# Kernel optimization log

Hardware: AMD Instinct MI355X
Metric: run time of the kernel (lower is better)

## Reference

```python
import jax, jax.numpy as jnp
import numpy as np

STEPS = 3


def setup_inputs() -> dict:
    key = jax.random.key(0)
    ks = jax.random.split(key, 6)
    N, H, B = 1000000, 128, 16384
    x = jax.random.normal(ks[0], (N, H), dtype=jnp.float32)
    batch_vec = jnp.sort(jax.random.randint(ks[1], (N,), 0, B)).astype(jnp.int64)
    scale_ih = 1.0 / np.sqrt(2 * H)
    scale_hh = 1.0 / np.sqrt(H)
    W_ih = jax.random.normal(ks[2], (4 * H, 2 * H), dtype=jnp.float32) * scale_ih
    W_hh = jax.random.normal(ks[3], (4 * H, H), dtype=jnp.float32) * scale_hh
    b_ih = jnp.zeros((4 * H,), dtype=jnp.float32)
    b_hh = jnp.zeros((4 * H,), dtype=jnp.float32)
    return {"x": x, "batch_vec": batch_vec, "W_ih": W_ih, "W_hh": W_hh,
            "b_ih": b_ih, "b_hh": b_hh, "num_graphs": B}


def _set2set(x, batch_vec, W_ih, W_hh, b_ih, b_hh, B):
    N, H = x.shape
    q_star = jnp.zeros((B, 2 * H), x.dtype)
    h = jnp.zeros((B, H), x.dtype)
    c = jnp.zeros((B, H), x.dtype)
    bias = b_ih + b_hh
    for _ in range(STEPS):
        # LSTMCell (torch gate order: i, f, g, o)
        gates = q_star @ W_ih.T + h @ W_hh.T + bias  # [B, 4H]
        i, f, g, o = jnp.split(gates, 4, axis=-1)
        c = jax.nn.sigmoid(f) * c + jax.nn.sigmoid(i) * jnp.tanh(g)
        h = jax.nn.sigmoid(o) * jnp.tanh(c)
        q = h  # [B, H]
        # attention logits per node
        e = jnp.sum(x * q[batch_vec], axis=-1)  # [N]
        emax = jax.ops.segment_max(e, batch_vec, num_segments=B)
        emax = jax.lax.stop_gradient(jnp.where(jnp.isfinite(emax), emax, 0.0))
        ex = jnp.exp(e - emax[batch_vec])
        denom = jax.ops.segment_sum(ex, batch_vec, num_segments=B)
        a = ex / denom[batch_vec]  # segment softmax, [N]
        r = jax.ops.segment_sum(a[:, None] * x, batch_vec, num_segments=B)  # [B, H]
        q_star = jnp.concatenate([q, r], axis=-1)  # [B, 2H]
    return q_star


def reference(x, batch_vec, W_ih, W_hh, b_ih, b_hh, num_graphs):
    return _set2set(x, batch_vec, W_ih, W_hh, b_ih, b_hh, int(num_graphs))
```

## Files before the change

kernel.cpp:

```cpp
#include <hip/hip_runtime.h>
#include <math.h>

#define HDIM 128
#define G4 512
#define TS 36

typedef float vf4 __attribute__((ext_vector_type(4)));
typedef unsigned short u16x8 __attribute__((ext_vector_type(8)));

__device__ __forceinline__ float sigm(float v) { return 1.0f / (1.0f + __expf(-v)); }
__device__ __forceinline__ float ftanh(float v) {
    return 1.0f - 2.0f / (__expf(2.0f * v) + 1.0f);
}
__device__ __forceinline__ float dot4(vf4 a, vf4 b) {
    return a.x * b.x + a.y * b.y + a.z * b.z + a.w * b.w;
}
__device__ __forceinline__ vf4 ldnt4(const float* p) {
    return __builtin_nontemporal_load((const vf4*)p);
}
__device__ __forceinline__ unsigned short f2bf(float f) {
    unsigned u = __float_as_uint(f);
    u += 0x7fff + ((u >> 16) & 1);
    return (unsigned short)(u >> 16);
}
__device__ __forceinline__ float bf2f(unsigned short h) {
    return __uint_as_float(((unsigned)h) << 16);
}

__global__ __launch_bounds__(256) void k_setup(const float* __restrict__ W_ih,
                                               const float* __restrict__ W_hh,
                                               const int* __restrict__ batch_vec, int N, int B,
                                               float* __restrict__ Wc, int* __restrict__ seg_start) {
    int t = blockIdx.x * 256 + threadIdx.x;
    if (t < G4 * 2 * HDIM) {
        int g = t >> 8;
        int k = t & 255;
        float w = W_ih[g * 256 + k];
        if (k < HDIM) w += W_hh[g * HDIM + k];
        Wc[t] = w;
    }
    if (t <= B) {
        int lo = 0, hi = N;
        while (lo < hi) {
            int mid = (lo + hi) >> 1;
            if (batch_vec[mid] < t) lo = mid + 1; else hi = mid;
        }
        seg_start[t] = lo;
    }
}

__global__ __launch_bounds__(256) void k_head(const float* __restrict__ Wc,
                                              const float* __restrict__ b_ih,
                                              const float* __restrict__ b_hh,
                                              float* __restrict__ gh0) {
    __shared__ float h0s[HDIM];
    int t = threadIdx.x;
    int g = blockIdx.x * 256 + t;
    if (t < HDIM) {
        float bi = b_ih[t] + b_hh[t];
        float bg = b_ih[2 * HDIM + t] + b_hh[2 * HDIM + t];
        float bo = b_ih[3 * HDIM + t] + b_hh[3 * HDIM + t];
        float c0 = sigm(bi) * ftanh(bg);
        h0s[t] = sigm(bo) * ftanh(c0);
    }
    __syncthreads();
    float s = 0.0f;
#pragma unroll
    for (int k = 0; k < HDIM; k += 4) {
        vf4 w = *(const vf4*)(Wc + (size_t)g * 256 + k);
        s += w.x * h0s[k] + w.y * h0s[k + 1] + w.z * h0s[k + 2] + w.w * h0s[k + 3];
    }
    gh0[g] = s;
}

#define UPD(m_, d_, ra_, rb_, p_, xa_, xb_)  \
    {                                        \
        float mn_ = fmaxf(m_, p_);           \
        float sc_ = __expf(m_ - mn_);        \
        float pe_ = __expf(p_ - mn_);        \
        d_ = d_ * sc_ + pe_;                 \
        ra_ = ra_ * sc_ + pe_ * xa_;         \
        rb_ = rb_ * sc_ + pe_ * xb_;         \
        m_ = mn_;                            \
    }

#define SHFL16(p_)                  \
    p_ += __shfl_xor(p_, 1, 64);    \
    p_ += __shfl_xor(p_, 2, 64);    \
    p_ += __shfl_xor(p_, 4, 64);    \
    p_ += __shfl_xor(p_, 8, 64);

#define MERGE_AND_WRITE()                                                     \
    {                                                                         \
        float M = fmaxf(m0, m1);                                              \
        float w0 = __expf(m0 - M), w1 = __expf(m1 - M);                       \
        d0 = d0 * w0 + d1 * w1;                                               \
        ra0 = ra0 * w0 + ra1 * w1;                                            \
        rb0 = rb0 * w0 + rb1 * w1;                                            \
        m0 = M;                                                               \
    }                                                                         \
    _Pragma("unroll")                                                         \
    for (int off = 16; off <= 32; off <<= 1) {                                \
        float om = __shfl_xor(m0, off, 64);                                   \
        float M = fmaxf(m0, om);                                              \
        float w = __expf(m0 - M);                                             \
        d0 *= w; ra0 *= w; rb0 *= w;                                          \
        d0 += __shfl_xor(d0, off, 64);                                        \
        ra0.x += __shfl_xor(ra0.x, off, 64);                                  \
        ra0.y += __shfl_xor(ra0.y, off, 64);                                  \
        ra0.z += __shfl_xor(ra0.z, off, 64);                                  \
        ra0.w += __shfl_xor(ra0.w, off, 64);                                  \
        rb0.x += __shfl_xor(rb0.x, off, 64);                                  \
        rb0.y += __shfl_xor(rb0.y, off, 64);                                  \
        rb0.z += __shfl_xor(rb0.z, off, 64);                                  \
        rb0.w += __shfl_xor(rb0.w, off, 64);                                  \
        m0 = M;                                                               \
    }                                                                         \
    float inv = (d0 > 0.0f) ? 1.0f / d0 : 0.0f;                               \
    if (quarter == 0) {                                                       \
        float* dst = r_out + (size_t)seg * ldr + col_off + l16 * 8;           \
        *(vf4*)dst = ra0 * inv;                                               \
        *(vf4*)(dst + 4) = rb0 * inv;                                         \
    }

__global__ __launch_bounds__(256) void k_attn_cvt(const float* __restrict__ x,
                                                  unsigned short* __restrict__ x16,
                                                  const float* __restrict__ b_ih,
                                                  const float* __restrict__ b_hh,
                                                  const int* __restrict__ seg_start,
                                                  float* __restrict__ r_out, int B) {
    const int ldr = HDIM, col_off = 0;
    int wave = threadIdx.x >> 6;
    int lane = threadIdx.x & 63;
    int l16 = lane & 15;
    int quarter = lane >> 4;
    int seg = (blockIdx.x << 2) + wave;
    if (seg >= B) return;
    int s = seg_start[seg], e = seg_start[seg + 1];

    vf4 qa, qb;
    {
        int c = l16 * 8;
        vf4 bi0 = *(const vf4*)(b_ih + c) + *(const vf4*)(b_hh + c);
        vf4 bi1 = *(const vf4*)(b_ih + c + 4) + *(const vf4*)(b_hh + c + 4);
        vf4 bg0 = *(const vf4*)(b_ih + 2 * HDIM + c) + *(const vf4*)(b_hh + 2 * HDIM + c);
        vf4 bg1 = *(const vf4*)(b_ih + 2 * HDIM + c + 4) + *(const vf4*)(b_hh + 2 * HDIM + c + 4);
        vf4 bo0 = *(const vf4*)(b_ih + 3 * HDIM + c) + *(const vf4*)(b_hh + 3 * HDIM + c);
        vf4 bo1 = *(const vf4*)(b_ih + 3 * HDIM + c + 4) + *(const vf4*)(b_hh + 3 * HDIM + c + 4);
#pragma unroll
        for (int j = 0; j < 4; ++j) {
            float c0 = sigm(bi0[j]) * ftanh(bg0[j]);
            qa[j] = sigm(bo0[j]) * ftanh(c0);
            float c1 = sigm(bi1[j]) * ftanh(bg1[j]);
            qb[j] = sigm(bo1[j]) * ftanh(c1);
        }
    }

    float m0 = 0.0f, d0 = 0.0f, m1 = 0.0f, d1 = 0.0f;
    vf4 ra0 = {0.f, 0.f, 0.f, 0.f}, rb0 = {0.f, 0.f, 0.f, 0.f};
    vf4 ra1 = {0.f, 0.f, 0.f, 0.f}, rb1 = {0.f, 0.f, 0.f, 0.f};

    int base = s;
#pragma unroll 1
    for (; base + 16 <= e; base += 16) {
        vf4 xa[4], xb[4];
        float p[4];
#pragma unroll
        for (int t = 0; t < 4; ++t) {
            const float* xr = x + (size_t)(base + quarter + 4 * t) * HDIM + l16 * 8;
            xa[t] = ldnt4(xr);
            xb[t] = ldnt4(xr + 4);
        }
#pragma unroll
        for (int t = 0; t < 4; ++t) {
            u16x8 cv;
            cv[0] = f2bf(xa[t].x); cv[1] = f2bf(xa[t].y); cv[2] = f2bf(xa[t].z); cv[3] = f2bf(xa[t].w);
            cv[4] = f2bf(xb[t].x); cv[5] = f2bf(xb[t].y); cv[6] = f2bf(xb[t].z); cv[7] = f2bf(xb[t].w);
            *(u16x8*)(x16 + (size_t)(base + quarter + 4 * t) * HDIM + l16 * 8) = cv;
            p[t] = dot4(xa[t], qa) + dot4(xb[t], qb);
        }
        SHFL16(p[0]) SHFL16(p[1]) SHFL16(p[2]) SHFL16(p[3])
        UPD(m0, d0, ra0, rb0, p[0], xa[0], xb[0])
        UPD(m1, d1, ra1, rb1, p[1], xa[1], xb[1])
        UPD(m0, d0, ra0, rb0, p[2], xa[2], xb[2])
        UPD(m1, d1, ra1, rb1, p[3], xa[3], xb[3])
    }
#pragma unroll 1
    for (; base < e; base += 4) {
        int row = base + quarter;
        int rl = min(row, e - 1);
        const float* xr = x + (size_t)rl * HDIM + l16 * 8;
        vf4 xa = ldnt4(xr), xb = ldnt4(xr + 4);
        u16x8 cv;
        cv[0] = f2bf(xa.x); cv[1] = f2bf(xa.y); cv[2] = f2bf(xa.z); cv[3] = f2bf(xa.w);
        cv[4] = f2bf(xb.x); cv[5] = f2bf(xb.y); cv[6] = f2bf(xb.z); cv[7] = f2bf(xb.w);
        *(u16x8*)(x16 + (size_t)rl * HDIM + l16 * 8) = cv;
        float p = dot4(xa, qa) + dot4(xb, qb);
        SHFL16(p)
        if (row >= e) p = -1e30f;
        UPD(m0, d0, ra0, rb0, p, xa, xb)
    }
    MERGE_AND_WRITE()
}

__global__ __launch_bounds__(256) void k_attn_b16(const unsigned short* __restrict__ x16,
                                                  const float* __restrict__ q,
                                                  const int* __restrict__ seg_start,
                                                  float* __restrict__ r_out, int ldr, int col_off,
                                                  int B, int rev) {
    int wave = threadIdx.x >> 6;
    int lane = threadIdx.x & 63;
    int l16 = lane & 15;
    int quarter = lane >> 4;
    int gid = (blockIdx.x << 2) + wave;
    if (gid >= B) return;
    int seg = rev ? (B - 1 - gid) : gid;
    int s = seg_start[seg], e = seg_start[seg + 1];

    const float* qrow = q + (size_t)seg * HDIM + l16 * 8;
    vf4 qa = *(const vf4*)qrow;
    vf4 qb = *(const vf4*)(qrow + 4);

    float m0 = 0.0f, d0 = 0.0f, m1 = 0.0f, d1 = 0.0f;
    vf4 ra0 = {0.f, 0.f, 0.f, 0.f}, rb0 = {0.f, 0.f, 0.f, 0.f};
    vf4 ra1 = {0.f, 0.f, 0.f, 0.f}, rb1 = {0.f, 0.f, 0.f, 0.f};

    int base = s;
#pragma unroll 1
    for (; base + 16 <= e; base += 16) {
        vf4 xa[4], xb[4];
        float p[4];
#pragma unroll
        for (int t = 0; t < 4; ++t) {
            const unsigned short* xr = x16 + (size_t)(base + quarter + 4 * t) * HDIM + l16 * 8;
            u16x8 u = *(const u16x8*)xr;
            xa[t] = vf4{bf2f(u[0]), bf2f(u[1]), bf2f(u[2]), bf2f(u[3])};
            xb[t] = vf4{bf2f(u[4]), bf2f(u[5]), bf2f(u[6]), bf2f(u[7])};
        }
#pragma unroll
        for (int t = 0; t < 4; ++t) p[t] = dot4(xa[t], qa) + dot4(xb[t], qb);
        SHFL16(p[0]) SHFL16(p[1]) SHFL16(p[2]) SHFL16(p[3])
        UPD(m0, d0, ra0, rb0, p[0], xa[0], xb[0])
        UPD(m1, d1, ra1, rb1, p[1], xa[1], xb[1])
        UPD(m0, d0, ra0, rb0, p[2], xa[2], xb[2])
        UPD(m1, d1, ra1, rb1, p[3], xa[3], xb[3])
    }
#pragma unroll 1
    for (; base < e; base += 4) {
        int row = base + quarter;
        const unsigned short* xr = x16 + (size_t)min(row, e - 1) * HDIM + l16 * 8;
        u16x8 u = *(const u16x8*)xr;
        vf4 xa = {bf2f(u[0]), bf2f(u[1]), bf2f(u[2]), bf2f(u[3])};
        vf4 xb = {bf2f(u[4]), bf2f(u[5]), bf2f(u[6]), bf2f(u[7])};
        float p = dot4(xa, qa) + dot4(xb, qb);
        SHFL16(p)
        if (row >= e) p = -1e30f;
        UPD(m0, d0, ra0, rb0, p, xa, xb)
    }
    MERGE_AND_WRITE()
}

__global__ __launch_bounds__(256) void k_gemm_lstm1(const float* __restrict__ r_prev,
                                                    const float* __restrict__ Wc,
                                                    const float* __restrict__ gh0,
                                                    const float* __restrict__ b_ih,
                                                    const float* __restrict__ b_hh,
                                                    float* __restrict__ h_new,
                                                    float* __restrict__ c_new) {
    __shared__ float As[128 * TS];
    __shared__ float Ws[64 * TS];
    int ct = blockIdx.y;
    int rb = blockIdx.x * 128;
    int tid = threadIdx.x;
    int tx = tid & 15, ty = tid >> 4;
    float acc[8][4];
#pragma unroll
    for (int i = 0; i < 8; ++i)
#pragma unroll
        for (int j = 0; j < 4; ++j) acc[i][j] = 0.0f;

    for (int kc = 0; kc < 4; ++kc) {
        int kbase = kc * 32;
#pragma unroll
        for (int i = 0; i < 4; ++i) {
            int li = tid + i * 256;
            int row = li >> 3;
            int c4 = (li & 7) * 4;
            *(vf4*)&As[row * TS + c4] = *(const vf4*)(r_prev + (size_t)(rb + row) * HDIM + kbase + c4);
        }
#pragma unroll
        for (int i = 0; i < 2; ++i) {
            int li = tid + i * 256;
            int col = li >> 3;
            int c4 = (li & 7) * 4;
            int g = ct * 16 + (col & 15) + 128 * (col >> 4);
            *(vf4*)&Ws[col * TS + c4] = *(const vf4*)(Wc + (size_t)g * 256 + 128 + kbase + c4);
        }
        __syncthreads();
#pragma unroll
        for (int k = 0; k < 32; k += 4) {
            vf4 a[8], b[4];
#pragma unroll
            for (int i = 0; i < 8; ++i) a[i] = *(vf4*)&As[(ty + 16 * i) * TS + k];
#pragma unroll
            for (int j = 0; j < 4; ++j) b[j] = *(vf4*)&Ws[(tx + 16 * j) * TS + k];
#pragma unroll
            for (int i = 0; i < 8; ++i)
#pragma unroll
                for (int j = 0; j < 4; ++j) {
                    acc[i][j] += a[i].x * b[j].x + a[i].y * b[j].y +
                                 a[i].z * b[j].z + a[i].w * b[j].w;
                }
        }
        __syncthreads();
    }
    int hidx = ct * 16 + tx;
    float bi = b_ih[hidx] + b_hh[hidx] + gh0[hidx];
    float bf = b_ih[HDIM + hidx] + b_hh[HDIM + hidx] + gh0[HDIM + hidx];
    float bg = b_ih[2 * HDIM + hidx] + b_hh[2 * HDIM + hidx] + gh0[2 * HDIM + hidx];
    float bo = b_ih[3 * HDIM + hidx] + b_hh[3 * HDIM + hidx] + gh0[3 * HDIM + hidx];
    float bi0 = b_ih[hidx] + b_hh[hidx];
    float bg0 = b_ih[2 * HDIM + hidx] + b_hh[2 * HDIM + hidx];
    float c0 = sigm(bi0) * ftanh(bg0);
#pragma unroll
    for (int i = 0; i < 8; ++i) {
        int row = rb + ty + 16 * i;
        float gi = acc[i][0] + bi;
        float gf = acc[i][1] + bf;
        float gg = acc[i][2] + bg;
        float go = acc[i][3] + bo;
        float cn = sigm(gf) * c0 + sigm(gi) * ftanh(gg);
        float hn = sigm(go) * ftanh(cn);
        c_new[(size_t)row * HDIM + hidx] = cn;
        h_new[(size_t)row * HDIM + hidx] = hn;
    }
}

__global__ __launch_bounds__(256) void k_gemm_lstm(const float* __restrict__ h_prev,
                                                   const float* __restrict__ r_prev,
                                                   const float* __restrict__ c_prev,
                                                   const float* __restrict__ Wc,
                                                   const float* __restrict__ b_ih,
                                                   const float* __restrict__ b_hh,
                                                   float* __restrict__ h_new,
                                                   float* __restrict__ c_new,
                                                   float* __restrict__ h_mirror) {
    __shared__ float As[128 * TS];
    __shared__ float Ws[64 * TS];
    int ct = blockIdx.y;
    int rb = blockIdx.x * 128;
    int tid = threadIdx.x;
    int tx = tid & 15, ty = tid >> 4;
    float acc[8][4];
#pragma unroll
    for (int i = 0; i < 8; ++i)
#pragma unroll
        for (int j = 0; j < 4; ++j) acc[i][j] = 0.0f;

    for (int kc = 0; kc < 8; ++kc) {
        const float* src = (kc < 4) ? h_prev : r_prev;
        int kbase = (kc & 3) * 32;
#pragma unroll
        for (int i = 0; i < 4; ++i) {
            int li = tid + i * 256;
            int row = li >> 3;
            int c4 = (li & 7) * 4;
            *(vf4*)&As[row * TS + c4] = *(const vf4*)(src + (size_t)(rb + row) * HDIM + kbase + c4);
        }
#pragma unroll
        for (int i = 0; i < 2; ++i) {
            int li = tid + i * 256;
            int col = li >> 3;
            int c4 = (li & 7) * 4;
            int g = ct * 16 + (col & 15) + 128 * (col >> 4);
            *(vf4*)&Ws[col * TS + c4] = *(const vf4*)(Wc + (size_t)g * 256 + kc * 32 + c4);
        }
        __syncthreads();
#pragma unroll
        for (int k = 0; k < 32; k += 4) {
            vf4 a[8], b[4];
#pragma unroll
            for (int i = 0; i < 8; ++i) a[i] = *(vf4*)&As[(ty + 16 * i) * TS + k];
#pragma unroll
            for (int j = 0; j < 4; ++j) b[j] = *(vf4*)&Ws[(tx + 16 * j) * TS + k];
#pragma unroll
            for (int i = 0; i < 8; ++i)
#pragma unroll
                for (int j = 0; j < 4; ++j) {
                    acc[i][j] += a[i].x * b[j].x + a[i].y * b[j].y +
                                 a[i].z * b[j].z + a[i].w * b[j].w;
                }
        }
        __syncthreads();
    }
    int hidx = ct * 16 + tx;
    float bi = b_ih[hidx] + b_hh[hidx];
    float bf = b_ih[HDIM + hidx] + b_hh[HDIM + hidx];
    float bg = b_ih[2 * HDIM + hidx] + b_hh[2 * HDIM + hidx];
    float bo = b_ih[3 * HDIM + hidx] + b_hh[3 * HDIM + hidx];
#pragma unroll
    for (int i = 0; i < 8; ++i) {
        int row = rb + ty + 16 * i;
        float gi = acc[i][0] + bi;
        float gf = acc[i][1] + bf;
        float gg = acc[i][2] + bg;
        float go = acc[i][3] + bo;
        float cp = c_prev[(size_t)row * HDIM + hidx];
        float cn = sigm(gf) * cp + sigm(gi) * ftanh(gg);
        float hn = sigm(go) * ftanh(cn);
        c_new[(size_t)row * HDIM + hidx] = cn;
        h_new[(size_t)row * HDIM + hidx] = hn;
        if (h_mirror) h_mirror[(size_t)row * 2 * HDIM + hidx] = hn;
    }
}

extern "C" void kernel_launch(void* const* d_in, const int* in_sizes, int n_in,
                              void* d_out, int out_size, void* d_ws, size_t ws_size,
                              hipStream_t stream) {
    const float* x = (const float*)d_in[0];
    const int* batch_vec = (const int*)d_in[1];
    const float* W_ih = (const float*)d_in[2];
    const float* W_hh = (const float*)d_in[3];
    const float* b_ih = (const float*)d_in[4];
    const float* b_hh = (const float*)d_in[5];
    float* out = (float*)d_out;

    int N = in_sizes[1];
    int B = out_size / (2 * HDIM);

    char* ws = (char*)d_ws;
    float* Wc = (float*)ws;            ws += (size_t)G4 * 2 * HDIM * 4;
    float* gh0 = (float*)ws;           ws += (size_t)G4 * 4;
    float* h_a = (float*)ws;           ws += (size_t)B * HDIM * 4;
    float* h_b = (float*)ws;           ws += (size_t)B * HDIM * 4;
    float* cbuf = (float*)ws;          ws += (size_t)B * HDIM * 4;
    float* rbuf = (float*)ws;          ws += (size_t)B * HDIM * 4;
    int* seg = (int*)ws;               ws += (size_t)(B + 1) * 4;
    ws = (char*)(((size_t)ws + 255) & ~(size_t)255);
    unsigned short* x16 = (unsigned short*)ws;

    k_setup<<<512, 256, 0, stream>>>(W_ih, W_hh, batch_vec, N, B, Wc, seg);
    k_head<<<2, 256, 0, stream>>>(Wc, b_ih, b_hh, gh0);

    dim3 ggrid(B / 128, 8);
    k_attn_cvt<<<(B + 3) / 4, 256, 0, stream>>>(x, x16, b_ih, b_hh, seg, rbuf, B);
    k_gemm_lstm1<<<ggrid, 256, 0, stream>>>(rbuf, Wc, gh0, b_ih, b_hh, h_b, cbuf);
    k_attn_b16<<<(B + 3) / 4, 256, 0, stream>>>(x16, h_b, seg, rbuf, HDIM, 0, B, 1);
    k_gemm_lstm<<<ggrid, 256, 0, stream>>>(h_b, rbuf, cbuf, Wc, b_ih, b_hh, h_a, cbuf, out);
    k_attn_b16<<<(B + 3) / 4, 256, 0, stream>>>(x16, h_a, seg, out, 2 * HDIM, HDIM, B, 0);
}
```

Baseline: 478.9 us.

## Split bf16 conversion into its own pass and remap attention blocks across XCDs

Moves the fp32-to-bf16 conversion of x out of the first attention pass into a standalone grid-stride kernel. All three attention passes now use one bf16 kernel with a block remap that gives each XCD a contiguous range of segments, in place of the reversed segment order used before. It also folds the gh0 head computation into the setup kernel and drops the unused h/c writes from the last LSTM step. The cost is that the first attention pass now reads bf16 x16 after a separate conversion pass, instead of fusing conversion with attention on fp32 x. That adds a full extra read of x16.

```diff
diff --git a/kernel.cpp b/kernel.cpp
--- a/kernel.cpp
+++ b/kernel.cpp
@@ -29,9 +29,35 @@
 
 __global__ __launch_bounds__(256) void k_setup(const float* __restrict__ W_ih,
                                                const float* __restrict__ W_hh,
+                                               const float* __restrict__ b_ih,
+                                               const float* __restrict__ b_hh,
                                                const int* __restrict__ batch_vec, int N, int B,
-                                               float* __restrict__ Wc, int* __restrict__ seg_start) {
+                                               float* __restrict__ Wc, int* __restrict__ seg_start,
+                                               float* __restrict__ gh0) {
+    __shared__ float h0s[HDIM];
     int t = blockIdx.x * 256 + threadIdx.x;
+    if (blockIdx.x < 2) {
+        if (threadIdx.x < HDIM) {
+            int hid = threadIdx.x;
+            float bi = b_ih[hid] + b_hh[hid];
+            float bg = b_ih[2 * HDIM + hid] + b_hh[2 * HDIM + hid];
+            float bo = b_ih[3 * HDIM + hid] + b_hh[3 * HDIM + hid];
+            float c0 = sigm(bi) * ftanh(bg);
+            h0s[hid] = sigm(bo) * ftanh(c0);
+        }
+        __syncthreads();
+        if (t < G4) {
+            float s = 0.0f;
+#pragma unroll
+            for (int k = 0; k < HDIM; k += 4) {
+                vf4 wi = *(const vf4*)(W_ih + (size_t)t * 256 + k);
+                vf4 wh = *(const vf4*)(W_hh + (size_t)t * HDIM + k);
+                s += (wi.x + wh.x) * h0s[k] + (wi.y + wh.y) * h0s[k + 1] +
+                     (wi.z + wh.z) * h0s[k + 2] + (wi.w + wh.w) * h0s[k + 3];
+            }
+            gh0[t] = s;
+        }
+    }
     if (t < G4 * 2 * HDIM) {
         int g = t >> 8;
         int k = t & 255;
@@ -49,28 +75,19 @@
     }
 }
 
-__global__ __launch_bounds__(256) void k_head(const float* __restrict__ Wc,
-                                              const float* __restrict__ b_ih,
-                                              const float* __restrict__ b_hh,
-                                              float* __restrict__ gh0) {
-    __shared__ float h0s[HDIM];
-    int t = threadIdx.x;
-    int g = blockIdx.x * 256 + t;
-    if (t < HDIM) {
-        float bi = b_ih[t] + b_hh[t];
-        float bg = b_ih[2 * HDIM + t] + b_hh[2 * HDIM + t];
-        float bo = b_ih[3 * HDIM + t] + b_hh[3 * HDIM + t];
-        float c0 = sigm(bi) * ftanh(bg);
-        h0s[t] = sigm(bo) * ftanh(c0);
-    }
-    __syncthreads();
-    float s = 0.0f;
-#pragma unroll
-    for (int k = 0; k < HDIM; k += 4) {
-        vf4 w = *(const vf4*)(Wc + (size_t)g * 256 + k);
-        s += w.x * h0s[k] + w.y * h0s[k + 1] + w.z * h0s[k + 2] + w.w * h0s[k + 3];
-    }
-    gh0[g] = s;
+__global__ __launch_bounds__(256) void k_cvt(const float* __restrict__ x,
+                                             unsigned short* __restrict__ x16,
+                                             long total8) {
+    long i = (long)blockIdx.x * 256 + threadIdx.x;
+    long stride = (long)gridDim.x * 256;
+    for (; i < total8; i += stride) {
+        vf4 a = ldnt4(x + i * 8);
+        vf4 b = ldnt4(x + i * 8 + 4);
+        u16x8 c;
+        c[0] = f2bf(a.x); c[1] = f2bf(a.y); c[2] = f2bf(a.z); c[3] = f2bf(a.w);
+        c[4] = f2bf(b.x); c[5] = f2bf(b.y); c[6] = f2bf(b.z); c[7] = f2bf(b.w);
+        *(u16x8*)(x16 + i * 8) = c;
+    }
 }
 
 #define UPD(m_, d_, ra_, rb_, p_, xa_, xb_)  \
@@ -90,56 +107,32 @@
     p_ += __shfl_xor(p_, 4, 64);    \
     p_ += __shfl_xor(p_, 8, 64);
 
-#define MERGE_AND_WRITE()                                                     \
-    {                                                                         \
-        float M = fmaxf(m0, m1);                                              \
-        float w0 = __expf(m0 - M), w1 = __expf(m1 - M);                       \
-        d0 = d0 * w0 + d1 * w1;                                               \
-        ra0 = ra0 * w0 + ra1 * w1;                                            \
-        rb0 = rb0 * w0 + rb1 * w1;                                            \
-        m0 = M;                                                               \
-    }                                                                         \
-    _Pragma("unroll")                                                         \
-    for (int off = 16; off <= 32; off <<= 1) {                                \
-        float om = __shfl_xor(m0, off, 64);                                   \
-        float M = fmaxf(m0, om);                                              \
-        float w = __expf(m0 - M);                                             \
-        d0 *= w; ra0 *= w; rb0 *= w;                                          \
-        d0 += __shfl_xor(d0, off, 64);                                        \
-        ra0.x += __shfl_xor(ra0.x, off, 64);                                  \
-        ra0.y += __shfl_xor(ra0.y, off, 64);                                  \
-        ra0.z += __shfl_xor(ra0.z, off, 64);                                  \
-        ra0.w += __shfl_xor(ra0.w, off, 64);                                  \
-        rb0.x += __shfl_xor(rb0.x, off, 64);                                  \
-        rb0.y += __shfl_xor(rb0.y, off, 64);                                  \
-        rb0.z += __shfl_xor(rb0.z, off, 64);                                  \
-        rb0.w += __shfl_xor(rb0.w, off, 64);                                  \
-        m0 = M;                                                               \
-    }                                                                         \
-    float inv = (d0 > 0.0f) ? 1.0f / d0 : 0.0f;                               \
-    if (quarter == 0) {                                                       \
-        float* dst = r_out + (size_t)seg * ldr + col_off + l16 * 8;           \
-        *(vf4*)dst = ra0 * inv;                                               \
-        *(vf4*)(dst + 4) = rb0 * inv;                                         \
-    }
-
-__global__ __launch_bounds__(256) void k_attn_cvt(const float* __restrict__ x,
-                                                  unsigned short* __restrict__ x16,
-                                                  const float* __restrict__ b_ih,
-                                                  const float* __restrict__ b_hh,
-                                                  const int* __restrict__ seg_start,
-                                                  float* __restrict__ r_out, int B) {
-    const int ldr = HDIM, col_off = 0;
+__global__ __launch_bounds__(256) void k_attn(const unsigned short* __restrict__ x16,
+                                              const float* __restrict__ q, int ldq,
+                                              const float* __restrict__ b_ih,
+                                              const float* __restrict__ b_hh,
+                                              const int* __restrict__ seg_start,
+                                              float* __restrict__ r_out, int ldr, int col_off,
+                                              int B) {
     int wave = threadIdx.x >> 6;
     int lane = threadIdx.x & 63;
     int l16 = lane & 15;
     int quarter = lane >> 4;
-    int seg = (blockIdx.x << 2) + wave;
+    int nblk = gridDim.x;
+    int bid = blockIdx.x;
+    int q8 = nblk >> 3, r8 = nblk & 7;
+    int xcd = bid & 7, pos = bid >> 3;
+    int nb = (xcd < r8 ? xcd * (q8 + 1) : r8 * (q8 + 1) + (xcd - r8) * q8) + pos;
+    int seg = (nb << 2) + wave;
     if (seg >= B) return;
     int s = seg_start[seg], e = seg_start[seg + 1];
 
     vf4 qa, qb;
-    {
+    if (q) {
+        const float* qrow = q + (size_t)seg * ldq + l16 * 8;
+        qa = *(const vf4*)qrow;
+        qb = *(const vf4*)(qrow + 4);
+    } else {
         int c = l16 * 8;
         vf4 bi0 = *(const vf4*)(b_ih + c) + *(const vf4*)(b_hh + c);
         vf4 bi1 = *(const vf4*)(b_ih + c + 4) + *(const vf4*)(b_hh + c + 4);
@@ -155,71 +148,6 @@
             qb[j] = sigm(bo1[j]) * ftanh(c1);
         }
     }
-
-    float m0 = 0.0f, d0 = 0.0f, m1 = 0.0f, d1 = 0.0f;
-    vf4 ra0 = {0.f, 0.f, 0.f, 0.f}, rb0 = {0.f, 0.f, 0.f, 0.f};
-    vf4 ra1 = {0.f, 0.f, 0.f, 0.f}, rb1 = {0.f, 0.f, 0.f, 0.f};
-
-    int base = s;
-#pragma unroll 1
-    for (; base + 16 <= e; base += 16) {
-        vf4 xa[4], xb[4];
-        float p[4];
-#pragma unroll
-        for (int t = 0; t < 4; ++t) {
-            const float* xr = x + (size_t)(base + quarter + 4 * t) * HDIM + l16 * 8;
-            xa[t] = ldnt4(xr);
-            xb[t] = ldnt4(xr + 4);
-        }
-#pragma unroll
-        for (int t = 0; t < 4; ++t) {
-            u16x8 cv;
-            cv[0] = f2bf(xa[t].x); cv[1] = f2bf(xa[t].y); cv[2] = f2bf(xa[t].z); cv[3] = f2bf(xa[t].w);
-            cv[4] = f2bf(xb[t].x); cv[5] = f2bf(xb[t].y); cv[6] = f2bf(xb[t].z); cv[7] = f2bf(xb[t].w);
-            *(u16x8*)(x16 + (size_t)(base + quarter + 4 * t) * HDIM + l16 * 8) = cv;
-            p[t] = dot4(xa[t], qa) + dot4(xb[t], qb);
-        }
-        SHFL16(p[0]) SHFL16(p[1]) SHFL16(p[2]) SHFL16(p[3])
-        UPD(m0, d0, ra0, rb0, p[0], xa[0], xb[0])
-        UPD(m1, d1, ra1, rb1, p[1], xa[1], xb[1])
-        UPD(m0, d0, ra0, rb0, p[2], xa[2], xb[2])
-        UPD(m1, d1, ra1, rb1, p[3], xa[3], xb[3])
-    }
-#pragma unroll 1
-    for (; base < e; base += 4) {
-        int row = base + quarter;
-        int rl = min(row, e - 1);
-        const float* xr = x + (size_t)rl * HDIM + l16 * 8;
-        vf4 xa = ldnt4(xr), xb = ldnt4(xr + 4);
-        u16x8 cv;
-        cv[0] = f2bf(xa.x); cv[1] = f2bf(xa.y); cv[2] = f2bf(xa.z); cv[3] = f2bf(xa.w);
-        cv[4] = f2bf(xb.x); cv[5] = f2bf(xb.y); cv[6] = f2bf(xb.z); cv[7] = f2bf(xb.w);
-        *(u16x8*)(x16 + (size_t)rl * HDIM + l16 * 8) = cv;
-        float p = dot4(xa, qa) + dot4(xb, qb);
-        SHFL16(p)
-        if (row >= e) p = -1e30f;
-        UPD(m0, d0, ra0, rb0, p, xa, xb)
-    }
-    MERGE_AND_WRITE()
-}
-
-__global__ __launch_bounds__(256) void k_attn_b16(const unsigned short* __restrict__ x16,
-                                                  const float* __restrict__ q,
-                                                  const int* __restrict__ seg_start,
-                                                  float* __restrict__ r_out, int ldr, int col_off,
-                                                  int B, int rev) {
-    int wave = threadIdx.x >> 6;
-    int lane = threadIdx.x & 63;
-    int l16 = lane & 15;
-    int quarter = lane >> 4;
-    int gid = (blockIdx.x << 2) + wave;
-    if (gid >= B) return;
-    int seg = rev ? (B - 1 - gid) : gid;
-    int s = seg_start[seg], e = seg_start[seg + 1];
-
-    const float* qrow = q + (size_t)seg * HDIM + l16 * 8;
-    vf4 qa = *(const vf4*)qrow;
-    vf4 qb = *(const vf4*)(qrow + 4);
 
     float m0 = 0.0f, d0 = 0.0f, m1 = 0.0f, d1 = 0.0f;
     vf4 ra0 = {0.f, 0.f, 0.f, 0.f}, rb0 = {0.f, 0.f, 0.f, 0.f};
@@ -257,7 +185,37 @@
         if (row >= e) p = -1e30f;
         UPD(m0, d0, ra0, rb0, p, xa, xb)
     }
-    MERGE_AND_WRITE()
+    {
+        float M = fmaxf(m0, m1);
+        float w0 = __expf(m0 - M), w1 = __expf(m1 - M);
+        d0 = d0 * w0 + d1 * w1;
+        ra0 = ra0 * w0 + ra1 * w1;
+        rb0 = rb0 * w0 + rb1 * w1;
+        m0 = M;
+    }
+#pragma unroll
+    for (int off = 16; off <= 32; off <<= 1) {
+        float om = __shfl_xor(m0, off, 64);
+        float M = fmaxf(m0, om);
+        float w = __expf(m0 - M);
+        d0 *= w; ra0 *= w; rb0 *= w;
+        d0 += __shfl_xor(d0, off, 64);
+        ra0.x += __shfl_xor(ra0.x, off, 64);
+        ra0.y += __shfl_xor(ra0.y, off, 64);
+        ra0.z += __shfl_xor(ra0.z, off, 64);
+        ra0.w += __shfl_xor(ra0.w, off, 64);
+        rb0.x += __shfl_xor(rb0.x, off, 64);
+        rb0.y += __shfl_xor(rb0.y, off, 64);
+        rb0.z += __shfl_xor(rb0.z, off, 64);
+        rb0.w += __shfl_xor(rb0.w, off, 64);
+        m0 = M;
+    }
+    float inv = (d0 > 0.0f) ? 1.0f / d0 : 0.0f;
+    if (quarter == 0) {
+        float* dst = r_out + (size_t)seg * ldr + col_off + l16 * 8;
+        *(vf4*)dst = ra0 * inv;
+        *(vf4*)(dst + 4) = rb0 * inv;
+    }
 }
 
 __global__ __launch_bounds__(256) void k_gemm_lstm1(const float* __restrict__ r_prev,
@@ -342,8 +300,6 @@
                                                    const float* __restrict__ Wc,
                                                    const float* __restrict__ b_ih,
                                                    const float* __restrict__ b_hh,
-                                                   float* __restrict__ h_new,
-                                                   float* __restrict__ c_new,
                                                    float* __restrict__ h_mirror) {
     __shared__ float As[128 * TS];
     __shared__ float Ws[64 * TS];
@@ -408,9 +364,7 @@
         float cp = c_prev[(size_t)row * HDIM + hidx];
         float cn = sigm(gf) * cp + sigm(gi) * ftanh(gg);
         float hn = sigm(go) * ftanh(cn);
-        c_new[(size_t)row * HDIM + hidx] = cn;
-        h_new[(size_t)row * HDIM + hidx] = hn;
-        if (h_mirror) h_mirror[(size_t)row * 2 * HDIM + hidx] = hn;
+        h_mirror[(size_t)row * 2 * HDIM + hidx] = hn;
     }
 }
 
@@ -431,7 +385,6 @@
     char* ws = (char*)d_ws;
     float* Wc = (float*)ws;            ws += (size_t)G4 * 2 * HDIM * 4;
     float* gh0 = (float*)ws;           ws += (size_t)G4 * 4;
-    float* h_a = (float*)ws;           ws += (size_t)B * HDIM * 4;
     float* h_b = (float*)ws;           ws += (size_t)B * HDIM * 4;
     float* cbuf = (float*)ws;          ws += (size_t)B * HDIM * 4;
     float* rbuf = (float*)ws;          ws += (size_t)B * HDIM * 4;
@@ -439,13 +392,14 @@
     ws = (char*)(((size_t)ws + 255) & ~(size_t)255);
     unsigned short* x16 = (unsigned short*)ws;
 
-    k_setup<<<512, 256, 0, stream>>>(W_ih, W_hh, batch_vec, N, B, Wc, seg);
-    k_head<<<2, 256, 0, stream>>>(Wc, b_ih, b_hh, gh0);
+    k_setup<<<512, 256, 0, stream>>>(W_ih, W_hh, b_ih, b_hh, batch_vec, N, B, Wc, seg, gh0);
+    k_cvt<<<2048, 256, 0, stream>>>(x, x16, (long)N * HDIM / 8);
 
     dim3 ggrid(B / 128, 8);
-    k_attn_cvt<<<(B + 3) / 4, 256, 0, stream>>>(x, x16, b_ih, b_hh, seg, rbuf, B);
+    int ablk = (B + 3) / 4;
+    k_attn<<<ablk, 256, 0, stream>>>(x16, nullptr, 0, b_ih, b_hh, seg, rbuf, HDIM, 0, B);
     k_gemm_lstm1<<<ggrid, 256, 0, stream>>>(rbuf, Wc, gh0, b_ih, b_hh, h_b, cbuf);
-    k_attn_b16<<<(B + 3) / 4, 256, 0, stream>>>(x16, h_b, seg, rbuf, HDIM, 0, B, 1);
-    k_gemm_lstm<<<ggrid, 256, 0, stream>>>(h_b, rbuf, cbuf, Wc, b_ih, b_hh, h_a, cbuf, out);
-    k_attn_b16<<<(B + 3) / 4, 256, 0, stream>>>(x16, h_a, seg, out, 2 * HDIM, HDIM, B, 0);
-}
+    k_attn<<<ablk, 256, 0, stream>>>(x16, h_b, HDIM, b_ih, b_hh, seg, rbuf, HDIM, 0, B);
+    k_gemm_lstm<<<ggrid, 256, 0, stream>>>(h_b, rbuf, cbuf, Wc, b_ih, b_hh, out);
+    k_attn<<<ablk, 256, 0, stream>>>(x16, out, 2 * HDIM, b_ih, b_hh, seg, out, 2 * HDIM, HDIM, B);
+}
```

Result: no change. 476.7 us (-0.5%).
